# Kernel tuning notes

Measured on AMD Instinct MI355X. Metric: run time of the kernel, lower is better.

Reference implementation:

```python
import jax, jax.numpy as jnp
import numpy as np

DIM = 768
HEADS = 12
HEAD_DIM = DIM // HEADS          # 64
DIM_HALF = HEAD_DIM // 2         # 32
SPATIAL = 3


def _rope_cos_sin(grid, voxel_size, theta):
    """grid: static tuple of ints (len SPATIAL); voxel_size: [SPATIAL] float;
    theta: [H, DIM_HALF] per-head frequency spectrum.
    Returns cos, sin of shape [H, N, DIM_HALF] where N = prod(grid)."""
    axes = [jnp.arange(g, dtype=theta.dtype) for g in grid]
    mesh = jnp.meshgrid(*axes, indexing='ij')
    coords = jnp.stack([m.reshape(-1) for m in mesh], axis=-1) * voxel_size  # [N, S] physical coords
    axis_idx = np.arange(DIM_HALF) % len(grid)        # round-robin freq->axis assignment
    pos = coords[:, axis_idx]                          # [N, DIM_HALF]
    ang = pos[None, :, :] * theta[:, None, :]          # [H, N, DIM_HALF]
    return jnp.cos(ang), jnp.sin(ang)


def _rope_apply(t, cos, sin):
    # t: [B, H, N, D]; cos/sin: [H, N, DIM_HALF] broadcast over batch
    t1, t2 = jnp.split(t, 2, axis=-1)
    return jnp.concatenate([t1 * cos - t2 * sin, t1 * sin + t2 * cos], axis=-1)


def setup_inputs() -> dict:
    key = jax.random.key(0)
    k_x, k_qkv, k_proj, k_b = jax.random.split(key, 4)
    B, N = 2, 8 * 16 * 16
    x = jax.random.normal(k_x, (B, N, DIM), dtype=jnp.float32)
    voxel_size = jnp.ones((SPATIAL,), dtype=jnp.float32)
    # nn.Linear weights are [out_features, in_features]
    w_qkv = jax.random.normal(k_qkv, (3 * DIM, DIM), dtype=jnp.float32) * (DIM ** -0.5)
    w_proj = jax.random.normal(k_proj, (DIM, DIM), dtype=jnp.float32) * (DIM ** -0.5)
    b_proj = jax.random.normal(k_b, (DIM,), dtype=jnp.float32) * 0.02
    # learnable per-head base frequencies: theta_j = 10000^{-j/dim_half}
    base = (1.0 / (10000.0 ** (np.arange(DIM_HALF, dtype=np.float32) / DIM_HALF)))
    theta = jnp.asarray(np.tile(base[None, :], (HEADS, 1)))  # [H, DIM_HALF]
    return {"x": x, "voxel_size": voxel_size, "w_qkv": w_qkv, "w_proj": w_proj,
            "b_proj": b_proj, "theta": theta, "grid_d": 8, "grid_h": 16, "grid_w": 16}


def reference(x, voxel_size, w_qkv, w_proj, b_proj, theta, grid_d, grid_h, grid_w):
    B, N, dim = x.shape
    H, D = HEADS, HEAD_DIM
    qkv = jnp.einsum('bnd,ed->bne', x, w_qkv).reshape(B, N, 3, H, D)
    qkv = jnp.transpose(qkv, (2, 0, 3, 1, 4))           # [3, B, H, N, D]
    q, k, v = qkv[0], qkv[1], qkv[2]
    cos, sin = _rope_cos_sin((grid_d, grid_h, grid_w), voxel_size, theta)
    q = _rope_apply(q, cos, sin)
    k = _rope_apply(k, cos, sin)
    scale = 1.0 / np.sqrt(D).astype(np.float32)
    attn = jax.nn.softmax(jnp.einsum('bhnd,bhmd->bhnm', q, k) * scale, axis=-1)
    out = jnp.einsum('bhnm,bhmd->bhnd', attn, v)        # [B, H, N, D]
    out = jnp.transpose(out, (0, 2, 1, 3)).reshape(B, N, dim)
    return out @ w_proj.T + b_proj
```

## Files before the change

kernel.cpp:

```cpp
#include <hip/hip_runtime.h>
#include <stdint.h>

#define DIM 768
#define NHEADS 12
#define HDIM 64
#define DHALF 32
#define NTOK 2048
#define LOG2E 1.44269504088896340736f

typedef unsigned short u16;
typedef unsigned int u32;
typedef __bf16 bf16x8 __attribute__((ext_vector_type(8)));
typedef short s16x8 __attribute__((ext_vector_type(8)));
typedef float f32x4 __attribute__((ext_vector_type(4)));

__device__ __forceinline__ f32x4 f4zero() { f32x4 z = {0.f, 0.f, 0.f, 0.f}; return z; }

__device__ __forceinline__ u16 f2bf(float f) {
    u32 u = __builtin_bit_cast(u32, f);
    u32 r = (u + 0x7FFFu + ((u >> 16) & 1u)) >> 16;
    return (u16)r;
}

__device__ __forceinline__ void gld_lds16(void* lds, const void* g) {
    __builtin_amdgcn_global_load_lds((const __attribute__((address_space(1))) u32*)g,
                                     (__attribute__((address_space(3))) u32*)lds,
                                     16, 0, 0);
}

__global__ __launch_bounds__(256) void cast3_f32_to_bf16(const float* __restrict__ a, u16* __restrict__ oa, int na4,
                                                         const float* __restrict__ b, u16* __restrict__ ob, int nb4,
                                                         const float* __restrict__ c, u16* __restrict__ oc, int nc4) {
    int i = blockIdx.x * 256 + threadIdx.x;
    const float* src;
    u16* dst;
    int j = i;
    if (i < na4) { src = a; dst = oa; }
    else if (i < na4 + nb4) { src = b; dst = ob; j = i - na4; }
    else if (i < na4 + nb4 + nc4) { src = c; dst = oc; j = i - na4 - nb4; }
    else return;
    float4 v = ((const float4*)src)[j];
    u32 w0 = (u32)f2bf(v.x) | ((u32)f2bf(v.y) << 16);
    u32 w1 = (u32)f2bf(v.z) | ((u32)f2bf(v.w) << 16);
    ((uint2*)dst)[j] = make_uint2(w0, w1);
}

__global__ __launch_bounds__(256) void gemm_bt(const u16* __restrict__ A, const u16* __restrict__ Bm,
                                               float* __restrict__ C, const float* __restrict__ bias,
                                               int M, int N, int K) {
    __shared__ __align__(16) u16 sA[128 * 32];
    __shared__ __align__(16) u16 sB[128 * 32];
    const int t = threadIdx.x;
    const int wave = t >> 6, lane = t & 63;
    const int quad = lane >> 4, l16 = lane & 15;
    const int bm = blockIdx.y * 128, bn = blockIdx.x * 128;
    const int wr = wave >> 1, wc = wave & 1;

    f32x4 acc[4][4];
#pragma unroll
    for (int i = 0; i < 4; i++)
#pragma unroll
        for (int j = 0; j < 4; j++) acc[i][j] = f4zero();

    for (int k0 = 0; k0 < K; k0 += 32) {
#pragma unroll
        for (int r = 0; r < 2; ++r) {
            int c = (r * 4 + wave) * 64 + lane;
            int row = c >> 2, kc = c & 3;
            gld_lds16((char*)sA + (size_t)(r * 4 + wave) * 1024,
                      A + (size_t)(bm + row) * K + k0 + kc * 8);
            gld_lds16((char*)sB + (size_t)(r * 4 + wave) * 1024,
                      Bm + (size_t)(bn + row) * K + k0 + kc * 8);
        }
        __syncthreads();
        bf16x8 af[4], bfr[4];
#pragma unroll
        for (int mb = 0; mb < 4; mb++)
            af[mb] = *(const bf16x8*)(sA + (wr * 64 + mb * 16 + l16) * 32 + quad * 8);
#pragma unroll
        for (int nb = 0; nb < 4; nb++)
            bfr[nb] = *(const bf16x8*)(sB + (wc * 64 + nb * 16 + l16) * 32 + quad * 8);
#pragma unroll
        for (int mb = 0; mb < 4; mb++)
#pragma unroll
            for (int nb = 0; nb < 4; nb++)
                acc[mb][nb] = __builtin_amdgcn_mfma_f32_16x16x32_bf16(af[mb], bfr[nb], acc[mb][nb], 0, 0, 0);
        __syncthreads();
    }
#pragma unroll
    for (int mb = 0; mb < 4; mb++)
#pragma unroll
        for (int nb = 0; nb < 4; nb++) {
            int col = bn + wc * 64 + nb * 16 + l16;
            float bv = bias ? bias[col] : 0.f;
#pragma unroll
            for (int r = 0; r < 4; r++) {
                int row = bm + wr * 64 + mb * 16 + quad * 4 + r;
                C[(size_t)row * N + col] = acc[mb][nb][r] + bv;
            }
        }
}

__global__ __launch_bounds__(256) void prep(const float* __restrict__ qkv,
                                            const float* __restrict__ voxel,
                                            const float* __restrict__ theta,
                                            const int* __restrict__ gh_p, const int* __restrict__ gw_p,
                                            u16* __restrict__ q_s, u16* __restrict__ k_s,
                                            u16* __restrict__ vT, int B, int nrope) {
    __shared__ u16 tile[64][66];
    int bid = blockIdx.x;
    int t = threadIdx.x;
    if (bid < nrope) {
        int tid = bid * 256 + t;
        int d = tid & (DHALF - 1);
        int n = (tid >> 5) & (NTOK - 1);
        int hb = tid >> 16;
        int h = hb % NHEADS;
        int b = hb / NHEADS;
        int gh = *gh_p, gw = *gw_p;
        int xw = n % gw;
        int rem = n / gw;
        int yh = rem % gh;
        int zd = rem / gh;
        int axis = d % 3;
        float coordv = (axis == 0 ? (float)zd : (axis == 1 ? (float)yh : (float)xw)) * voxel[axis];
        float ang = coordv * theta[h * DHALF + d];
        float s, c;
        __sincosf(ang, &s, &c);
        size_t bi = ((size_t)b * NTOK + n) * (3 * DIM);
        const float* qp = qkv + bi + h * HDIM;
        float q1 = qp[d], q2 = qp[d + DHALF];
        float k1 = qp[DIM + d], k2 = qp[DIM + d + DHALF];
        size_t bh = (size_t)b * NHEADS + h;
        size_t bo = (bh * NTOK + n) * HDIM;
        const float qscale = 0.125f * LOG2E;
        q_s[bo + d] = f2bf((q1 * c - q2 * s) * qscale);
        q_s[bo + d + DHALF] = f2bf((q1 * s + q2 * c) * qscale);
        int tile_i = n >> 6, r = n & 63, g = r >> 4, k16 = r & 15;
        int qd = d >> 3, j = d & 7;
        size_t off = bh * NTOK * HDIM + (size_t)tile_i * 4096 +
                     (size_t)(g * 2) * 512 + (qd * 16 + k16) * 8 + j;
        k_s[off] = f2bf(k1 * c - k2 * s);
        k_s[off + 512] = f2bf(k1 * s + k2 * c);
    } else {
        int idx = bid - nrope;
        int nt = idx & 31;
        int rem = idx >> 5;
        int h = rem % NHEADS, b = rem / NHEADS;
        int n_loc = t >> 2, d0 = (t & 3) * 16;
        const float* src = qkv + ((size_t)b * NTOK + nt * 64 + n_loc) * (3 * DIM) + 2 * DIM + h * HDIM + d0;
#pragma unroll
        for (int j = 0; j < 16; j += 4) {
            float4 v = *(const float4*)(src + j);
            tile[n_loc][d0 + j + 0] = f2bf(v.x);
            tile[n_loc][d0 + j + 1] = f2bf(v.y);
            tile[n_loc][d0 + j + 2] = f2bf(v.z);
            tile[n_loc][d0 + j + 3] = f2bf(v.w);
        }
        __syncthreads();
        int db = t >> 6, l = t & 63, q = (t >> 4) & 3, l16 = t & 15;
        int dd = db * 16 + l16;
        size_t bh = (size_t)b * NHEADS + h;
#pragma unroll
        for (int c = 0; c < 2; c++) {
            u32 w[4];
#pragma unroll
            for (int jp = 0; jp < 4; jp++) {
                int jj0 = jp * 2, jj1 = jp * 2 + 1;
                int key0 = c * 32 + (jj0 < 4 ? 4 * q + jj0 : 16 + 4 * q + jj0 - 4);
                int key1 = c * 32 + (jj1 < 4 ? 4 * q + jj1 : 16 + 4 * q + jj1 - 4);
                w[jp] = (u32)tile[key0][dd] | ((u32)tile[key1][dd] << 16);
            }
            u16* dst = vT + ((bh * 64 + (size_t)nt * 2 + c) * 2048 + db * 512 + (size_t)l * 8);
            *(uint4*)dst = make_uint4(w[0], w[1], w[2], w[3]);
        }
    }
}

__global__ __launch_bounds__(256) void flash_attn(const u16* __restrict__ Q, const u16* __restrict__ Kp,
                                                  const u16* __restrict__ Vp, u16* __restrict__ Out, int NBH) {
    int i = blockIdx.x;
    int bh_i = i % NBH;
    int qt = i / NBH;
    int b = bh_i / NHEADS, h = bh_i % NHEADS;
    int t = threadIdx.x, wave = t >> 6, lane = t & 63, quad = lane >> 4, l16 = lane & 15;
    size_t bh = (size_t)b * NHEADS + h;
    const u16* Qb = Q + bh * NTOK * HDIM;
    const u16* Kb = Kp + bh * NTOK * HDIM;
    const u16* Vb = Vp + bh * NTOK * HDIM;

    __shared__ __align__(16) u16 smem[2][8192];

    const int q0 = qt * 128 + wave * 32;
    bf16x8 qf[2][2];
#pragma unroll
    for (int qb = 0; qb < 2; qb++)
#pragma unroll
        for (int kc = 0; kc < 2; kc++)
            qf[qb][kc] = *(const bf16x8*)(Qb + (size_t)(q0 + qb * 16 + l16) * HDIM + kc * 32 + quad * 8);

    s16x8 ov;
#pragma unroll
    for (int j = 0; j < 8; j++) ov[j] = (l16 == 0) ? (short)0x3F80 : (short)0;

    f32x4 o[2][5];
#pragma unroll
    for (int qb = 0; qb < 2; qb++)
#pragma unroll
        for (int db = 0; db < 5; db++) o[qb][db] = f4zero();

    auto stage = [&](int kt, int bi) {
        const u16* Kg = Kb + (size_t)kt * 4096;
        const u16* Vg = Vb + (size_t)kt * 4096;
        u16* buf = &smem[bi][0];
#pragma unroll
        for (int s = 0; s < 2; s++) {
            gld_lds16(buf + (wave * 2 + s) * 512, Kg + (wave * 2 + s) * 512 + lane * 8);
            gld_lds16(buf + 4096 + (wave * 2 + s) * 512, Vg + (wave * 2 + s) * 512 + lane * 8);
        }
    };

    stage(0, 0);
    int cur = 0;
    for (int kt = 0; kt < NTOK / 64; ++kt) {
        __syncthreads();
        if (kt + 1 < NTOK / 64) stage(kt + 1, cur ^ 1);
        const u16* sK = &smem[cur][0];
        const u16* sV = &smem[cur][4096];
#pragma unroll
        for (int c = 0; c < 2; ++c) {
            bf16x8 kf[2][2];
#pragma unroll
            for (int kb2 = 0; kb2 < 2; kb2++)
#pragma unroll
                for (int kc = 0; kc < 2; kc++)
                    kf[kb2][kc] = *(const bf16x8*)(sK + ((c * 2 + kb2) * 2 + kc) * 512 + lane * 8);
            s16x8 bv[4];
#pragma unroll
            for (int db = 0; db < 4; db++)
                bv[db] = *(const s16x8*)(sV + c * 2048 + db * 512 + lane * 8);
#pragma unroll
            for (int qb = 0; qb < 2; qb++) {
                f32x4 st0, st1;
                {
                    f32x4 z = f4zero();
                    z = __builtin_amdgcn_mfma_f32_16x16x32_bf16(kf[0][0], qf[qb][0], z, 0, 0, 0);
                    st0 = __builtin_amdgcn_mfma_f32_16x16x32_bf16(kf[0][1], qf[qb][1], z, 0, 0, 0);
                    f32x4 z2 = f4zero();
                    z2 = __builtin_amdgcn_mfma_f32_16x16x32_bf16(kf[1][0], qf[qb][0], z2, 0, 0, 0);
                    st1 = __builtin_amdgcn_mfma_f32_16x16x32_bf16(kf[1][1], qf[qb][1], z2, 0, 0, 0);
                }
                bf16x8 pb;
#pragma unroll
                for (int r = 0; r < 4; r++) {
                    pb[r] = (__bf16)__builtin_exp2f(st0[r]);
                    pb[r + 4] = (__bf16)__builtin_exp2f(st1[r]);
                }
#pragma unroll
                for (int db = 0; db < 4; db++)
                    o[qb][db] = __builtin_amdgcn_mfma_f32_16x16x32_bf16(pb, __builtin_bit_cast(bf16x8, bv[db]),
                                                                       o[qb][db], 0, 0, 0);
                o[qb][4] = __builtin_amdgcn_mfma_f32_16x16x32_bf16(pb, __builtin_bit_cast(bf16x8, ov),
                                                                  o[qb][4], 0, 0, 0);
            }
        }
        cur ^= 1;
    }

#pragma unroll
    for (int qb = 0; qb < 2; qb++)
#pragma unroll
        for (int r = 0; r < 4; r++) {
            float s = __shfl(o[qb][4][r], lane & 48);
            float inv = 1.0f / s;
            int n = q0 + qb * 16 + quad * 4 + r;
            u16* dst = Out + ((size_t)b * NTOK + n) * DIM + h * HDIM + l16;
#pragma unroll
            for (int db = 0; db < 4; db++)
                dst[db * 16] = f2bf(o[qb][db][r] * inv);
        }
}

extern "C" void kernel_launch(void* const* d_in, const int* in_sizes, int n_in,
                              void* d_out, int out_size, void* d_ws, size_t ws_size,
                              hipStream_t stream) {
    const float* x = (const float*)d_in[0];
    const float* voxel = (const float*)d_in[1];
    const float* w_qkv = (const float*)d_in[2];
    const float* w_proj = (const float*)d_in[3];
    const float* b_proj = (const float*)d_in[4];
    const float* theta = (const float*)d_in[5];
    const int* gh_p = (const int*)d_in[7];
    const int* gw_p = (const int*)d_in[8];
    const int B = in_sizes[0] / (NTOK * DIM);
    const int M = B * NTOK;

    char* p = (char*)d_ws;
    u16* xb = (u16*)p;       p += (size_t)M * DIM * 2;
    u16* wqkvb = (u16*)p;    p += (size_t)3 * DIM * DIM * 2;
    u16* wprojb = (u16*)p;   p += (size_t)DIM * DIM * 2;
    float* qkv = (float*)p;  p += (size_t)M * 3 * DIM * 4;
    u16* q_s = (u16*)p;      p += (size_t)M * DIM * 2;
    u16* k_s = (u16*)p;      p += (size_t)M * DIM * 2;
    u16* vT = (u16*)p;       p += (size_t)M * DIM * 2;
    u16* attn = (u16*)p;     p += (size_t)M * DIM * 2;

    int na4 = M * DIM / 4, nb4 = 3 * DIM * DIM / 4, nc4 = DIM * DIM / 4;
    cast3_f32_to_bf16<<<dim3((na4 + nb4 + nc4 + 255) / 256), 256, 0, stream>>>(
        x, xb, na4, w_qkv, wqkvb, nb4, w_proj, wprojb, nc4);

    gemm_bt<<<dim3(3 * DIM / 128, M / 128), 256, 0, stream>>>(xb, wqkvb, qkv, nullptr, M, 3 * DIM, DIM);

    int nrope = (B * NHEADS * NTOK * DHALF) / 256;
    int nvt = B * NHEADS * (NTOK / 64);
    prep<<<dim3(nrope + nvt), 256, 0, stream>>>(qkv, voxel, theta, gh_p, gw_p, q_s, k_s, vT, B, nrope);

    flash_attn<<<dim3((B * NHEADS * NTOK) / 128), 256, 0, stream>>>(q_s, k_s, vT, attn, B * NHEADS);

    gemm_bt<<<dim3(DIM / 128, M / 128), 256, 0, stream>>>(attn, wprojb, (float*)d_out, b_proj, M, DIM, DIM);
}
```

Baseline: 204.9 us.

## Split flash attention key tiles across wave pairs and merge partial outputs in LDS

Each block's four waves become a 2x2 grid. Each wave pair owns 64 query rows and each wave handles half of every 64-key tile, so a wave processes 4 query blocks over 32 keys instead of 2 query blocks over 64 keys. This reuses each K/V fragment read from LDS across more queries and cuts per-wave LDS traffic. In exchange it needs more accumulator registers and adds an LDS reduction of the partial outputs and row sums, with extra barriers, at the end. The unnormalized exp without a max makes the split-K merge a simple sum.

```diff
diff --git a/kernel.cpp b/kernel.cpp
--- a/kernel.cpp
+++ b/kernel.cpp
@@ -184,17 +184,19 @@
     int qt = i / NBH;
     int b = bh_i / NHEADS, h = bh_i % NHEADS;
     int t = threadIdx.x, wave = t >> 6, lane = t & 63, quad = lane >> 4, l16 = lane & 15;
+    const int wr = wave >> 1, wc = wave & 1;
     size_t bh = (size_t)b * NHEADS + h;
     const u16* Qb = Q + bh * NTOK * HDIM;
     const u16* Kb = Kp + bh * NTOK * HDIM;
     const u16* Vb = Vp + bh * NTOK * HDIM;
 
-    __shared__ __align__(16) u16 smem[2][8192];
-
-    const int q0 = qt * 128 + wave * 32;
-    bf16x8 qf[2][2];
-#pragma unroll
-    for (int qb = 0; qb < 2; qb++)
+    __shared__ __align__(16) u16 stg[2][8192];
+    __shared__ __align__(16) float pub[2][64][68];
+
+    const int q0 = qt * 128 + wr * 64;
+    bf16x8 qf[4][2];
+#pragma unroll
+    for (int qb = 0; qb < 4; qb++)
 #pragma unroll
         for (int kc = 0; kc < 2; kc++)
             qf[qb][kc] = *(const bf16x8*)(Qb + (size_t)(q0 + qb * 16 + l16) * HDIM + kc * 32 + quad * 8);
@@ -203,16 +205,16 @@
 #pragma unroll
     for (int j = 0; j < 8; j++) ov[j] = (l16 == 0) ? (short)0x3F80 : (short)0;
 
-    f32x4 o[2][5];
-#pragma unroll
-    for (int qb = 0; qb < 2; qb++)
+    f32x4 o[4][5];
+#pragma unroll
+    for (int qb = 0; qb < 4; qb++)
 #pragma unroll
         for (int db = 0; db < 5; db++) o[qb][db] = f4zero();
 
     auto stage = [&](int kt, int bi) {
         const u16* Kg = Kb + (size_t)kt * 4096;
         const u16* Vg = Vb + (size_t)kt * 4096;
-        u16* buf = &smem[bi][0];
+        u16* buf = &stg[bi][0];
 #pragma unroll
         for (int s = 0; s < 2; s++) {
             gld_lds16(buf + (wave * 2 + s) * 512, Kg + (wave * 2 + s) * 512 + lane * 8);
@@ -225,60 +227,76 @@
     for (int kt = 0; kt < NTOK / 64; ++kt) {
         __syncthreads();
         if (kt + 1 < NTOK / 64) stage(kt + 1, cur ^ 1);
-        const u16* sK = &smem[cur][0];
-        const u16* sV = &smem[cur][4096];
-#pragma unroll
-        for (int c = 0; c < 2; ++c) {
-            bf16x8 kf[2][2];
-#pragma unroll
-            for (int kb2 = 0; kb2 < 2; kb2++)
-#pragma unroll
-                for (int kc = 0; kc < 2; kc++)
-                    kf[kb2][kc] = *(const bf16x8*)(sK + ((c * 2 + kb2) * 2 + kc) * 512 + lane * 8);
-            s16x8 bv[4];
+        const u16* sK = &stg[cur][0];
+        const u16* sV = &stg[cur][4096];
+        bf16x8 kf[2][2];
+#pragma unroll
+        for (int kb2 = 0; kb2 < 2; kb2++)
+#pragma unroll
+            for (int kc = 0; kc < 2; kc++)
+                kf[kb2][kc] = *(const bf16x8*)(sK + ((wc * 2 + kb2) * 2 + kc) * 512 + lane * 8);
+        s16x8 bv[4];
+#pragma unroll
+        for (int db = 0; db < 4; db++)
+            bv[db] = *(const s16x8*)(sV + wc * 2048 + db * 512 + lane * 8);
+#pragma unroll
+        for (int qb = 0; qb < 4; qb++) {
+            f32x4 st0, st1;
+            {
+                f32x4 z = f4zero();
+                z = __builtin_amdgcn_mfma_f32_16x16x32_bf16(kf[0][0], qf[qb][0], z, 0, 0, 0);
+                st0 = __builtin_amdgcn_mfma_f32_16x16x32_bf16(kf[0][1], qf[qb][1], z, 0, 0, 0);
+                f32x4 z2 = f4zero();
+                z2 = __builtin_amdgcn_mfma_f32_16x16x32_bf16(kf[1][0], qf[qb][0], z2, 0, 0, 0);
+                st1 = __builtin_amdgcn_mfma_f32_16x16x32_bf16(kf[1][1], qf[qb][1], z2, 0, 0, 0);
+            }
+            bf16x8 pb;
+#pragma unroll
+            for (int r = 0; r < 4; r++) {
+                pb[r] = (__bf16)__builtin_exp2f(st0[r]);
+                pb[r + 4] = (__bf16)__builtin_exp2f(st1[r]);
+            }
 #pragma unroll
             for (int db = 0; db < 4; db++)
-                bv[db] = *(const s16x8*)(sV + c * 2048 + db * 512 + lane * 8);
-#pragma unroll
-            for (int qb = 0; qb < 2; qb++) {
-                f32x4 st0, st1;
-                {
-                    f32x4 z = f4zero();
-                    z = __builtin_amdgcn_mfma_f32_16x16x32_bf16(kf[0][0], qf[qb][0], z, 0, 0, 0);
-                    st0 = __builtin_amdgcn_mfma_f32_16x16x32_bf16(kf[0][1], qf[qb][1], z, 0, 0, 0);
-                    f32x4 z2 = f4zero();
-                    z2 = __builtin_amdgcn_mfma_f32_16x16x32_bf16(kf[1][0], qf[qb][0], z2, 0, 0, 0);
-                    st1 = __builtin_amdgcn_mfma_f32_16x16x32_bf16(kf[1][1], qf[qb][1], z2, 0, 0, 0);
+                o[qb][db] = __builtin_amdgcn_mfma_f32_16x16x32_bf16(pb, __builtin_bit_cast(bf16x8, bv[db]),
+                                                                   o[qb][db], 0, 0, 0);
+            o[qb][4] = __builtin_amdgcn_mfma_f32_16x16x32_bf16(pb, __builtin_bit_cast(bf16x8, ov),
+                                                              o[qb][4], 0, 0, 0);
+        }
+        cur ^= 1;
+    }
+
+    __syncthreads();
+    if (wc == 1) {
+#pragma unroll
+        for (int qb = 0; qb < 4; qb++)
+#pragma unroll
+            for (int r = 0; r < 4; r++) {
+                int row = qb * 16 + quad * 4 + r;
+#pragma unroll
+                for (int db = 0; db < 4; db++)
+                    pub[wr][row][db * 16 + l16] = o[qb][db][r];
+                if (l16 == 0) pub[wr][row][64] = o[qb][4][r];
+            }
+    }
+    __syncthreads();
+    if (wc == 0) {
+#pragma unroll
+        for (int qb = 0; qb < 4; qb++)
+#pragma unroll
+            for (int r = 0; r < 4; r++) {
+                int row = qb * 16 + quad * 4 + r;
+                float stot = __shfl(o[qb][4][r], lane & 48) + pub[wr][row][64];
+                float inv = 1.0f / stot;
+                int n = q0 + row;
+                u16* dst = Out + ((size_t)b * NTOK + n) * DIM + h * HDIM + l16;
+#pragma unroll
+                for (int db = 0; db < 4; db++) {
+                    float val = o[qb][db][r] + pub[wr][row][db * 16 + l16];
+                    dst[db * 16] = f2bf(val * inv);
                 }
-                bf16x8 pb;
-#pragma unroll
-                for (int r = 0; r < 4; r++) {
-                    pb[r] = (__bf16)__builtin_exp2f(st0[r]);
-                    pb[r + 4] = (__bf16)__builtin_exp2f(st1[r]);
-                }
-#pragma unroll
-                for (int db = 0; db < 4; db++)
-                    o[qb][db] = __builtin_amdgcn_mfma_f32_16x16x32_bf16(pb, __builtin_bit_cast(bf16x8, bv[db]),
-                                                                       o[qb][db], 0, 0, 0);
-                o[qb][4] = __builtin_amdgcn_mfma_f32_16x16x32_bf16(pb, __builtin_bit_cast(bf16x8, ov),
-                                                                  o[qb][4], 0, 0, 0);
-            }
-        }
-        cur ^= 1;
-    }
-
-#pragma unroll
-    for (int qb = 0; qb < 2; qb++)
-#pragma unroll
-        for (int r = 0; r < 4; r++) {
-            float s = __shfl(o[qb][4][r], lane & 48);
-            float inv = 1.0f / s;
-            int n = q0 + qb * 16 + quad * 4 + r;
-            u16* dst = Out + ((size_t)b * NTOK + n) * DIM + h * HDIM + l16;
-#pragma unroll
-            for (int db = 0; db < 4; db++)
-                dst[db * 16] = f2bf(o[qb][db][r] * inv);
-        }
+            }
+    }
 }
 
 extern "C" void kernel_launch(void* const* d_in, const int* in_sizes, int n_in,
```

Result: slower. 213.6 us (+4.2%).
